# Kernel optimization log

Measured on AMD Instinct MI355X. Metric: run time of the kernel, lower is better.

## Reference

```python
import jax, jax.numpy as jnp
import numpy as np

# Fixed geometry from the module's voxel_dict
VOXEL = np.array([0.32, 0.32, 6.0], dtype=np.float32)
PC_MIN = np.array([-74.88, -74.88, -2.0], dtype=np.float32)
PC_MAX = np.array([74.88, 74.88, 4.0], dtype=np.float32)
NX, NY, NZ = 468, 468, 1          # round((max-min)/voxel) per axis
CANVAS = NZ * NY * NX             # 219024 voxels (batch_size = 1)
OFFSET = VOXEL / 2.0 + PC_MIN     # x/y/z_offset from __init__


def setup_inputs() -> dict:
    key = jax.random.key(0)
    k1, k2, k3, k4 = jax.random.split(key, 4)
    N = 400000
    # points uniformly inside the point-cloud range (dynamic voxelization keeps all)
    xyz = jax.random.uniform(k1, (N, 3), dtype=jnp.float32) * (PC_MAX - PC_MIN) * 0.999 + PC_MIN
    extra = jax.random.normal(k2, (N, 2), dtype=jnp.float32)
    points = jnp.concatenate([xyz, extra], axis=1)          # [N, 5]
    W1 = jax.random.normal(k3, (11, 64), dtype=jnp.float32) * 0.05
    W2 = jax.random.normal(k4, (128, 64), dtype=jnp.float32) * 0.05
    return {"points": points, "W1": W1, "W2": W2}


def _flat_voxel_index(xyz):
    # dynamic voxelization: integer voxel coord per point, (z, y, x) ordering
    c = jnp.floor((xyz - PC_MIN) / VOXEL).astype(jnp.int32)
    cx = jnp.clip(c[:, 0], 0, NX - 1)
    cy = jnp.clip(c[:, 1], 0, NY - 1)
    cz = jnp.clip(c[:, 2], 0, NZ - 1)
    flat = cz * (NY * NX) + cy * NX + cx                    # canvas index as in map_voxel_center_to_point
    return flat, cx, cy, cz


def reference(points, W1, W2):
    xyz = points[:, :3]
    flat, cx, cy, cz = _flat_voxel_index(xyz)

    # DynamicScatter mean (cluster_scatter)
    cnt = jax.ops.segment_sum(jnp.ones((points.shape[0],), jnp.float32), flat, num_segments=CANVAS)
    vsum = jax.ops.segment_sum(points, flat, num_segments=CANVAS)
    vmean = vsum / jnp.maximum(cnt, 1.0)[:, None]           # [CANVAS, 5]
    pmean = vmean[flat]                                     # gather voxel mean to points

    f_cluster = xyz - pmean[:, :3]
    centers = jnp.stack([cx, cy, cz], axis=1).astype(jnp.float32) * VOXEL + OFFSET
    f_center = xyz - centers
    features = jnp.concatenate([points, f_cluster, f_center], axis=-1)   # [N, 11]

    occ = (cnt > 0)[:, None]

    # PFN layer 1: Linear(bias=False) + ReLU, then scatter-max to voxels
    pf1 = jax.nn.relu(features @ W1)                        # [N, 64]
    v1 = jax.ops.segment_max(pf1, flat, num_segments=CANVAS)
    v1 = jnp.where(occ, v1, 0.0)                            # zero empty voxels (replaces -inf)

    # gather voxel max back to points, concat, PFN layer 2
    feat2 = jnp.concatenate([pf1, v1[flat]], axis=1)        # [N, 128]
    pf2 = jax.nn.relu(feat2 @ W2)                           # [N, 64]
    v2 = jax.ops.segment_max(pf2, flat, num_segments=CANVAS)
    v2 = jnp.where(occ, v2, 0.0)                            # [CANVAS, 64] dense voxel features
    return v2
```

## Files before the change

kernel.cpp:

```cpp
#include <hip/hip_runtime.h>

#define NXc 468
#define NYc 468
#define CANVASc (468 * 468)
#define NPTS 400000
#define RUN 16
#define NRUNS (NPTS / RUN)
#define GPTS ((NPTS + 255) / 256)
#define GVOX ((CANVASc + 255) / 256)
#define GBND (NRUNS / 4)

#define PCMIN_X (-74.88f)
#define PCMIN_Y (-74.88f)
#define VOX_X 0.32f
#define VOX_Y 0.32f
#define OFF_X (-74.72f)
#define OFF_Y (-74.72f)
#define OFF_Z (1.0f)

typedef __attribute__((ext_vector_type(8))) short v8s;
typedef __attribute__((ext_vector_type(4))) float v4f;

static_assert(sizeof(__bf16) == 2, "bf16 must be 2 bytes");

__device__ __forceinline__ int rli(int x, int p) {
    return __builtin_amdgcn_readlane(x, p);
}
__device__ __forceinline__ float rlf(float x, int p) {
    return __int_as_float(__builtin_amdgcn_readlane(__float_as_int(x), p));
}

__device__ __forceinline__ void split8(const float* f, v8s& h, v8s& l) {
    #pragma unroll
    for (int i = 0; i < 8; i += 2) {
        __bf16 h0 = (__bf16)f[i];
        __bf16 h1 = (__bf16)f[i + 1];
        h[i]     = __builtin_bit_cast(short, h0);
        h[i + 1] = __builtin_bit_cast(short, h1);
        float l0 = f[i]     - (float)h0;
        float l1 = f[i + 1] - (float)h1;
        l[i]     = __builtin_bit_cast(short, (__bf16)l0);
        l[i + 1] = __builtin_bit_cast(short, (__bf16)l1);
    }
}

__device__ __forceinline__ int voxel_cell(float x, float y, int& cx, int& cy) {
    cx = (int)floorf((x - PCMIN_X) / VOX_X);
    cy = (int)floorf((y - PCMIN_Y) / VOX_Y);
    cx = min(max(cx, 0), NXc - 1);
    cy = min(max(cy, 0), NYc - 1);
    return cy * NXc + cx;
}

__device__ __forceinline__ void kw_body(int tid,
                                        const float* __restrict__ W1,
                                        const float* __restrict__ W2,
                                        v8s* __restrict__ w1frag,
                                        v8s* __restrict__ w2frag) {
    if (tid < 1024) {
        int f = tid >> 6, lane = tid & 63;
        int t = f >> 2, c = f & 3;
        int q = lane >> 4, n = lane & 15;
        float v[8];
        #pragma unroll
        for (int i = 0; i < 8; i++) v[i] = W2[(c * 32 + q * 8 + i) * 64 + t * 16 + n];
        v8s h, l;
        split8(v, h, l);
        w2frag[(f * 2 + 0) * 64 + lane] = h;
        w2frag[(f * 2 + 1) * 64 + lane] = l;
    } else if (tid < 1280) {
        int f = (tid - 1024) >> 6, lane = (tid - 1024) & 63;
        int q = lane >> 4, n = lane & 15;
        float v[8];
        #pragma unroll
        for (int i = 0; i < 8; i++) {
            int k = q * 8 + i;
            v[i] = (k < 11) ? W1[k * 64 + f * 16 + n] : 0.f;
        }
        v8s h, l;
        split8(v, h, l);
        w1frag[(f * 2 + 0) * 64 + lane] = h;
        w1frag[(f * 2 + 1) * 64 + lane] = l;
    }
}

__global__ __launch_bounds__(256) void k_stats(const float* __restrict__ pts,
                                               int* __restrict__ cnt,
                                               int* __restrict__ rankb,
                                               int* __restrict__ cellu,
                                               const float* __restrict__ W1,
                                               const float* __restrict__ W2,
                                               v8s* __restrict__ w1frag,
                                               v8s* __restrict__ w2frag) {
    int b = blockIdx.x;
    if (b >= GPTS) {
        kw_body((b - GPTS) * 256 + threadIdx.x, W1, W2, w1frag, w2frag);
        return;
    }
    int i = b * 256 + threadIdx.x;
    if (i >= NPTS) return;
    float x = pts[i * 5 + 0], y = pts[i * 5 + 1];
    int cx, cy;
    int fl = voxel_cell(x, y, cx, cy);
    rankb[i] = atomicAdd(&cnt[fl], 1);
    cellu[i] = cx | (cy << 16);
}

__global__ __launch_bounds__(256) void k_alloc(const int* __restrict__ cnt,
                                               int* __restrict__ cursor,
                                               int* __restrict__ gcur) {
    int v = blockIdx.x * 256 + threadIdx.x;
    int lane = threadIdx.x & 63;
    int c = (v < CANVASc) ? cnt[v] : 0;
    int scan = c;
    #pragma unroll
    for (int off = 1; off < 64; off <<= 1) {
        int t = __shfl_up(scan, off, 64);
        if (lane >= off) scan += t;
    }
    int total = __shfl(scan, 63, 64);
    int base = 0;
    if (lane == 0 && total > 0) base = atomicAdd(gcur, total);
    base = __shfl(base, 0, 64);
    if (v < CANVASc) cursor[v] = base + scan - c;
}

__device__ __forceinline__ void gather_pt(const float* __restrict__ pts, int pi,
                                          float4& A, float& e1) {
    const float* pp = pts + (size_t)pi * 5;
    __builtin_memcpy(&A, pp, 16);
    e1 = pp[4];
}

__global__ __launch_bounds__(256) void k_scatter(const float* __restrict__ pts,
                                                 const int* __restrict__ cursor,
                                                 const int* __restrict__ rankb,
                                                 const int* __restrict__ cellu,
                                                 float4* __restrict__ pos4,
                                                 float* __restrict__ e1b,
                                                 int* __restrict__ cellb) {
    int i = blockIdx.x * 256 + threadIdx.x;
    if (i >= NPTS) return;
    float4 A; float e1;
    gather_pt(pts, i, A, e1);
    int cell = cellu[i];
    int cx = cell & 0xFFFF, cy = cell >> 16;
    int fl = cy * NXc + cx;
    int pos = cursor[fl] + rankb[i];
    pos4[pos] = A;
    e1b[pos] = e1;
    cellb[pos] = cell;
}

__global__ __launch_bounds__(256) void kV(const int* __restrict__ cnt,
                                          const int* __restrict__ cursor,
                                          const float4* __restrict__ pos4,
                                          const float* __restrict__ e1b,
                                          const int* __restrict__ cellb,
                                          const float* __restrict__ W1,
                                          float4* __restrict__ vmean4,
                                          float* __restrict__ v1c,
                                          float* __restrict__ out) {
    int b = blockIdx.x;
    if (b >= GVOX) {
        int j = threadIdx.x & 63;
        int wslot = threadIdx.x >> 6;
        int w = (b - GVOX) * 4 + wslot;
        if (w == 0 || w >= NRUNS) return;
        int bb = w * RUN;
        int ca = cellb[bb - 1], cb0 = cellb[bb];
        if (ca != cb0) return;
        int cx = ca & 0xFFFF, cy = ca >> 16;
        int v = cy * NXc + cx;
        int c = cnt[v];
        int start = cursor[v];
        out[(size_t)v * 64 + j] = 0.f;

        float sx = 0.f, sy = 0.f, sz = 0.f;
        for (int pb = 0; pb < c; pb += 64) {
            int pc = min(c - pb, 64);
            if (j < pc) {
                float4 A = pos4[start + pb + j];
                sx += A.x; sy += A.y; sz += A.z;
            }
        }
        #pragma unroll
        for (int off = 1; off < 64; off <<= 1) {
            sx += __shfl_xor(sx, off, 64);
            sy += __shfl_xor(sy, off, 64);
            sz += __shfl_xor(sz, off, 64);
        }
        float inv = 1.0f / (float)c;
        float mx = sx * inv, my = sy * inv, mz = sz * inv;

        float wgt[11];
        #pragma unroll
        for (int k = 0; k < 11; k++) wgt[k] = W1[k * 64 + j];
        float vmax = 0.f;
        for (int pb = 0; pb < c; pb += 64) {
            int pc = min(c - pb, 64);
            float f[11];
            #pragma unroll
            for (int k = 0; k < 11; k++) f[k] = 0.f;
            if (j < pc) {
                int idx = start + pb + j;
                float4 A = pos4[idx];
                float e1 = e1b[idx];
                int cell = cellb[idx];
                int ccx = cell & 0xFFFF, ccy = cell >> 16;
                f[0] = A.x; f[1] = A.y; f[2] = A.z; f[3] = A.w; f[4] = e1;
                f[5] = A.x - mx; f[6] = A.y - my; f[7] = A.z - mz;
                f[8] = A.x - (ccx * VOX_X + OFF_X);
                f[9] = A.y - (ccy * VOX_Y + OFF_Y);
                f[10] = A.z - OFF_Z;
            }
            for (int p = 0; p < pc; p++) {
                float acc = 0.f;
                #pragma unroll
                for (int k = 0; k < 11; k++)
                    acc = fmaf(rlf(f[k], p), wgt[k], acc);
                vmax = fmaxf(vmax, acc);
            }
        }
        v1c[(size_t)w * 64 + j] = vmax;
        return;
    }
    int v = b * 256 + threadIdx.x;
    if (v >= CANVASc) return;
    int c = cnt[v];
    if (c == 0) {
        float4 z = make_float4(0.f, 0.f, 0.f, 0.f);
        float4* o = (float4*)out + (size_t)v * 16;
        #pragma unroll
        for (int i = 0; i < 16; i++) o[i] = z;
        return;
    }
    int start = cursor[v];
    float sx = 0.f, sy = 0.f, sz = 0.f;
    for (int i = 0; i < c; i++) {
        float4 p = pos4[start + i];
        sx += p.x; sy += p.y; sz += p.z;
    }
    float inv = 1.0f / (float)c;
    vmean4[v] = make_float4(sx * inv, sy * inv, sz * inv, 0.f);
}

struct PtRegs {
    float4 A;
    float  e1, fcx, fcy, fcz;
    float  mx, my, mz;
    int    vx;
};
__device__ __forceinline__ PtRegs load_pt(const float4* __restrict__ pos4,
                                          const float* __restrict__ e1b,
                                          const int* __restrict__ cellb,
                                          const float4* __restrict__ vmean4,
                                          int base, int j) {
    PtRegs r;
    r.A = make_float4(0.f, 0.f, 0.f, 0.f);
    r.e1 = r.fcx = r.fcy = r.fcz = r.mx = r.my = r.mz = 0.f;
    r.vx = -1;
    int idx = -1;
    if (j < RUN) idx = base + j;
    else if (j == 16) idx = (base + RUN < NPTS) ? base + RUN : -1;
    else if (j == 17) idx = base - 1;
    if (idx >= 0) {
        int cell = cellb[idx];
        int cx = cell & 0xFFFF, cy = cell >> 16;
        int vv = cy * NXc + cx;
        r.vx = vv;
        if (j < RUN) {
            float4 A = pos4[idx];
            r.A = A;
            r.e1 = e1b[idx];
            r.fcx = A.x - (cx * VOX_X + OFF_X);
            r.fcy = A.y - (cy * VOX_Y + OFF_Y);
            r.fcz = A.z - OFF_Z;
            float4 m = vmean4[vv];
            r.mx = m.x; r.my = m.y; r.mz = m.z;
        }
    }
    return r;
}

#define PSTR 68

__device__ __forceinline__ void phase1_mfma(float (*s_pf)[PSTR], const PtRegs& P,
                                            const v8s* __restrict__ w1frag, int j) {
    if (j < RUN) {
        float* row = s_pf[j];
        row[0] = P.A.x; row[1] = P.A.y; row[2] = P.A.z; row[3] = P.A.w; row[4] = P.e1;
        row[5] = P.A.x - P.mx; row[6] = P.A.y - P.my; row[7] = P.A.z - P.mz;
        row[8] = P.fcx; row[9] = P.fcy; row[10] = P.fcz;
        #pragma unroll
        for (int t = 11; t < 16; t++) row[t] = 0.f;
    }
    __builtin_amdgcn_wave_barrier();

    const int m = j & 15, q = j >> 4;
    v8s fh = {0,0,0,0,0,0,0,0}, fl_ = {0,0,0,0,0,0,0,0};
    if (q < 2) {
        float f8[8];
        #pragma unroll
        for (int i = 0; i < 8; i++) f8[i] = s_pf[m][q * 8 + i];
        split8(f8, fh, fl_);
    }
    v4f d[4];
    #pragma unroll
    for (int t = 0; t < 4; t++) {
        v8s bh = w1frag[(t * 2 + 0) * 64 + j];
        v8s bl = w1frag[(t * 2 + 1) * 64 + j];
        v4f acc = {0.f, 0.f, 0.f, 0.f};
        acc = __builtin_amdgcn_mfma_f32_16x16x32_bf16(fh,  bh, acc, 0, 0, 0);
        acc = __builtin_amdgcn_mfma_f32_16x16x32_bf16(fl_, bh, acc, 0, 0, 0);
        acc = __builtin_amdgcn_mfma_f32_16x16x32_bf16(fh,  bl, acc, 0, 0, 0);
        d[t] = acc;
    }
    __builtin_amdgcn_wave_barrier();
    #pragma unroll
    for (int t = 0; t < 4; t++)
        #pragma unroll
        for (int r = 0; r < 4; r++)
            s_pf[q * 4 + r][t * 16 + m] = fmaxf(d[t][r], 0.f);
    __builtin_amdgcn_wave_barrier();
}

__global__ __launch_bounds__(256) void kB(const float4* __restrict__ pos4,
                                          const float* __restrict__ e1b,
                                          const int* __restrict__ cellb,
                                          const float4* __restrict__ vmean4,
                                          const v8s* __restrict__ w1frag,
                                          const v8s* __restrict__ w2frag,
                                          const float* __restrict__ v1c,
                                          float* __restrict__ out) {
    __shared__ float s_pf[4][RUN][PSTR];
    int wslot = threadIdx.x >> 6;
    int wave = blockIdx.x * 4 + wslot;
    int j = threadIdx.x & 63;
    int base = wave * RUN;

    PtRegs P = load_pt(pos4, e1b, cellb, vmean4, base, j);

    const int m = j & 15, q = j >> 4;

    const int first = rli(P.vx, 0), last = rli(P.vx, RUN - 1);
    const bool firstExt = (rli(P.vx, 17) == first);
    const bool lastExt  = (rli(P.vx, 16) == last);

    int vx_m = __builtin_amdgcn_ds_bpermute(m << 2, P.vx);
    int vx_prev = __shfl_up(P.vx, 1, 64);
    unsigned long long B =
        __ballot((j < RUN) && ((j == 0) || (P.vx != vx_prev)));
    int s_seg = 63 - __builtin_clzll(B & ((2ULL << m) - 1ULL));
    int e_seg = m + 1 + (int)__builtin_ctzll((B | (1ULL << RUN)) >> (m + 1));
    const bool fext_m = (vx_m == first && firstExt);
    const bool ext_m = fext_m || (vx_m == last && lastExt);
    const int bidx = fext_m ? wave : (wave + 1);

    phase1_mfma(s_pf[wslot], P, w1frag, j);

    float vf[16];
    if (ext_m) {
        const float* vr = v1c + (size_t)bidx * 64 + q * 8;
        #pragma unroll
        for (int c = 0; c < 2; c++)
            #pragma unroll
            for (int i = 0; i < 8; i++) vf[c * 8 + i] = vr[c * 32 + i];
    }

    v8s ah[4], al[4];
    #pragma unroll
    for (int c = 0; c < 2; c++) {
        float f[8];
        #pragma unroll
        for (int i = 0; i < 8; i++) f[i] = s_pf[wslot][m][c * 32 + q * 8 + i];
        split8(f, ah[c], al[c]);
    }
    if (!ext_m) {
        #pragma unroll
        for (int i = 0; i < 16; i++) vf[i] = 0.f;
        for (int p = s_seg; p < e_seg; p++) {
            const float* row = s_pf[wslot][p];
            float4 a0 = *(const float4*)&row[q * 8];
            float4 a1 = *(const float4*)&row[q * 8 + 4];
            float4 b0 = *(const float4*)&row[32 + q * 8];
            float4 b1 = *(const float4*)&row[32 + q * 8 + 4];
            vf[0] = fmaxf(vf[0], a0.x);  vf[1] = fmaxf(vf[1], a0.y);
            vf[2] = fmaxf(vf[2], a0.z);  vf[3] = fmaxf(vf[3], a0.w);
            vf[4] = fmaxf(vf[4], a1.x);  vf[5] = fmaxf(vf[5], a1.y);
            vf[6] = fmaxf(vf[6], a1.z);  vf[7] = fmaxf(vf[7], a1.w);
            vf[8] = fmaxf(vf[8], b0.x);  vf[9] = fmaxf(vf[9], b0.y);
            vf[10] = fmaxf(vf[10], b0.z); vf[11] = fmaxf(vf[11], b0.w);
            vf[12] = fmaxf(vf[12], b1.x); vf[13] = fmaxf(vf[13], b1.y);
            vf[14] = fmaxf(vf[14], b1.z); vf[15] = fmaxf(vf[15], b1.w);
        }
    }
    split8(vf + 0, ah[2], al[2]);
    split8(vf + 8, ah[3], al[3]);
    __builtin_amdgcn_wave_barrier();

    #pragma unroll
    for (int t = 0; t < 4; t++) {
        v8s bh[4], bl[4];
        #pragma unroll
        for (int c = 0; c < 4; c++) {
            bh[c] = w2frag[((t * 4 + c) * 2 + 0) * 64 + j];
            bl[c] = w2frag[((t * 4 + c) * 2 + 1) * 64 + j];
        }
        v4f acc = {0.f, 0.f, 0.f, 0.f};
        #pragma unroll
        for (int c = 0; c < 4; c++) {
            acc = __builtin_amdgcn_mfma_f32_16x16x32_bf16(ah[c], bh[c], acc, 0, 0, 0);
            acc = __builtin_amdgcn_mfma_f32_16x16x32_bf16(al[c], bh[c], acc, 0, 0, 0);
            acc = __builtin_amdgcn_mfma_f32_16x16x32_bf16(ah[c], bl[c], acc, 0, 0, 0);
        }
        #pragma unroll
        for (int r = 0; r < 4; r++) s_pf[wslot][q * 4 + r][t * 16 + m] = acc[r];
    }
    __builtin_amdgcn_wave_barrier();

    int vprev = first;
    float smax = -3.4e38f;
    for (int p = 0; p < RUN; p++) {
        int vp = rli(P.vx, p);
        if (vp != vprev) {
            float r = fmaxf(smax, 0.f);
            size_t o = (size_t)vprev * 64 + j;
            bool ua = (vprev == first && firstExt) || (vprev == last && lastExt);
            if (ua) atomicMax((int*)out + o, __float_as_int(r));
            else out[o] = r;
            vprev = vp; smax = -3.4e38f;
        }
        smax = fmaxf(smax, s_pf[wslot][p][j]);
    }
    {
        float r = fmaxf(smax, 0.f);
        size_t o = (size_t)vprev * 64 + j;
        bool ua = (vprev == first && firstExt) || (vprev == last && lastExt);
        if (ua) atomicMax((int*)out + o, __float_as_int(r));
        else out[o] = r;
    }
}

extern "C" void kernel_launch(void* const* d_in, const int* in_sizes, int n_in,
                              void* d_out, int out_size, void* d_ws, size_t ws_size,
                              hipStream_t stream) {
    const float* pts = (const float*)d_in[0];
    const float* W1  = (const float*)d_in[1];
    const float* W2  = (const float*)d_in[2];
    float* out = (float*)d_out;

    float4* vmean4 = (float4*)d_ws;
    float*  v1c    = (float*)(vmean4 + CANVASc);
    float4* pos4   = (float4*)(v1c + (size_t)NRUNS * 64);
    float*  e1b    = (float*)(pos4 + NPTS);
    int*    cellb  = (int*)(e1b + NPTS);
    int*    rankb  = cellb + NPTS;
    int*    cellu  = rankb + NPTS;
    v8s*    w2frag = (v8s*)(cellu + NPTS);
    v8s*    w1frag = w2frag + 2048;
    int*    cnt    = (int*)(w1frag + 512);
    int*    gcur   = cnt + CANVASc;
    int*    cursor = gcur + 1;

    hipMemsetAsync(cnt, 0, (size_t)(CANVASc + 1) * 4, stream);

    k_stats  <<<GPTS + 5, 256, 0, stream>>>(pts, cnt, rankb, cellu,
                                            W1, W2, w1frag, w2frag);
    k_alloc  <<<GVOX, 256, 0, stream>>>(cnt, cursor, gcur);
    k_scatter<<<GPTS, 256, 0, stream>>>(pts, cursor, rankb, cellu,
                                        pos4, e1b, cellb);
    kV       <<<GVOX + GBND, 256, 0, stream>>>(cnt, cursor, pos4, e1b, cellb,
                                               W1, vmean4, v1c, out);
    kB       <<<NRUNS / 4, 256, 0, stream>>>(pos4, e1b, cellb, vmean4, w1frag,
                                             w2frag, v1c, out);
}
```

Measured before the change: 221.8 us.

## Compute voxel means in-wave in kB and move empty-voxel zeroing into k_alloc

The per-voxel mean pass over the whole canvas is removed. kB now computes each voxel's mean from the run's points using wave shuffles over segment bounds. Only voxels that span run boundaries get their mean precomputed, by the boundary kernel, into a small per-run buffer. Zeroing of empty voxels' output moves into k_alloc, so the old kV kernel shrinks to a boundary-only kernel. This removes a canvas-wide read/write of vmean4 and a random gather, in exchange for extra shuffle work in kB.

```diff
diff --git a/kernel.cpp b/kernel.cpp
--- a/kernel.cpp
+++ b/kernel.cpp
@@ -108,7 +108,8 @@
 
 __global__ __launch_bounds__(256) void k_alloc(const int* __restrict__ cnt,
                                                int* __restrict__ cursor,
-                                               int* __restrict__ gcur) {
+                                               int* __restrict__ gcur,
+                                               float4* __restrict__ out4) {
     int v = blockIdx.x * 256 + threadIdx.x;
     int lane = threadIdx.x & 63;
     int c = (v < CANVASc) ? cnt[v] : 0;
@@ -122,7 +123,15 @@
     int base = 0;
     if (lane == 0 && total > 0) base = atomicAdd(gcur, total);
     base = __shfl(base, 0, 64);
-    if (v < CANVASc) cursor[v] = base + scan - c;
+    if (v < CANVASc) {
+        cursor[v] = base + scan - c;
+        if (c == 0) {
+            float4 z = make_float4(0.f, 0.f, 0.f, 0.f);
+            float4* o = out4 + (size_t)v * 16;
+            #pragma unroll
+            for (int i = 0; i < 16; i++) o[i] = z;
+        }
+    }
 }
 
 __device__ __forceinline__ void gather_pt(const float* __restrict__ pts, int pi,
@@ -152,97 +161,76 @@
     cellb[pos] = cell;
 }
 
-__global__ __launch_bounds__(256) void kV(const int* __restrict__ cnt,
+__global__ __launch_bounds__(256) void kS(const int* __restrict__ cnt,
                                           const int* __restrict__ cursor,
                                           const float4* __restrict__ pos4,
                                           const float* __restrict__ e1b,
                                           const int* __restrict__ cellb,
                                           const float* __restrict__ W1,
-                                          float4* __restrict__ vmean4,
+                                          float4* __restrict__ vmc,
                                           float* __restrict__ v1c,
                                           float* __restrict__ out) {
-    int b = blockIdx.x;
-    if (b >= GVOX) {
-        int j = threadIdx.x & 63;
-        int wslot = threadIdx.x >> 6;
-        int w = (b - GVOX) * 4 + wslot;
-        if (w == 0 || w >= NRUNS) return;
-        int bb = w * RUN;
-        int ca = cellb[bb - 1], cb0 = cellb[bb];
-        if (ca != cb0) return;
-        int cx = ca & 0xFFFF, cy = ca >> 16;
-        int v = cy * NXc + cx;
-        int c = cnt[v];
-        int start = cursor[v];
-        out[(size_t)v * 64 + j] = 0.f;
-
-        float sx = 0.f, sy = 0.f, sz = 0.f;
-        for (int pb = 0; pb < c; pb += 64) {
-            int pc = min(c - pb, 64);
-            if (j < pc) {
-                float4 A = pos4[start + pb + j];
-                sx += A.x; sy += A.y; sz += A.z;
-            }
-        }
-        #pragma unroll
-        for (int off = 1; off < 64; off <<= 1) {
-            sx += __shfl_xor(sx, off, 64);
-            sy += __shfl_xor(sy, off, 64);
-            sz += __shfl_xor(sz, off, 64);
-        }
-        float inv = 1.0f / (float)c;
-        float mx = sx * inv, my = sy * inv, mz = sz * inv;
-
-        float wgt[11];
-        #pragma unroll
-        for (int k = 0; k < 11; k++) wgt[k] = W1[k * 64 + j];
-        float vmax = 0.f;
-        for (int pb = 0; pb < c; pb += 64) {
-            int pc = min(c - pb, 64);
-            float f[11];
+    int j = threadIdx.x & 63;
+    int wslot = threadIdx.x >> 6;
+    int w = blockIdx.x * 4 + wslot;
+    if (w == 0 || w >= NRUNS) return;
+    int bb = w * RUN;
+    int ca = cellb[bb - 1], cb0 = cellb[bb];
+    if (ca != cb0) return;
+    int cx = ca & 0xFFFF, cy = ca >> 16;
+    int v = cy * NXc + cx;
+    int c = cnt[v];
+    int start = cursor[v];
+    out[(size_t)v * 64 + j] = 0.f;
+
+    float sx = 0.f, sy = 0.f, sz = 0.f;
+    for (int pb = 0; pb < c; pb += 64) {
+        int pc = min(c - pb, 64);
+        if (j < pc) {
+            float4 A = pos4[start + pb + j];
+            sx += A.x; sy += A.y; sz += A.z;
+        }
+    }
+    #pragma unroll
+    for (int off = 1; off < 64; off <<= 1) {
+        sx += __shfl_xor(sx, off, 64);
+        sy += __shfl_xor(sy, off, 64);
+        sz += __shfl_xor(sz, off, 64);
+    }
+    float inv = 1.0f / (float)c;
+    float mx = sx * inv, my = sy * inv, mz = sz * inv;
+    if (j == 0) vmc[w] = make_float4(mx, my, mz, 0.f);
+
+    float wgt[11];
+    #pragma unroll
+    for (int k = 0; k < 11; k++) wgt[k] = W1[k * 64 + j];
+    float vmax = 0.f;
+    for (int pb = 0; pb < c; pb += 64) {
+        int pc = min(c - pb, 64);
+        float f[11];
+        #pragma unroll
+        for (int k = 0; k < 11; k++) f[k] = 0.f;
+        if (j < pc) {
+            int idx = start + pb + j;
+            float4 A = pos4[idx];
+            float e1 = e1b[idx];
+            int cell = cellb[idx];
+            int ccx = cell & 0xFFFF, ccy = cell >> 16;
+            f[0] = A.x; f[1] = A.y; f[2] = A.z; f[3] = A.w; f[4] = e1;
+            f[5] = A.x - mx; f[6] = A.y - my; f[7] = A.z - mz;
+            f[8] = A.x - (ccx * VOX_X + OFF_X);
+            f[9] = A.y - (ccy * VOX_Y + OFF_Y);
+            f[10] = A.z - OFF_Z;
+        }
+        for (int p = 0; p < pc; p++) {
+            float acc = 0.f;
             #pragma unroll
-            for (int k = 0; k < 11; k++) f[k] = 0.f;
-            if (j < pc) {
-                int idx = start + pb + j;
-                float4 A = pos4[idx];
-                float e1 = e1b[idx];
-                int cell = cellb[idx];
-                int ccx = cell & 0xFFFF, ccy = cell >> 16;
-                f[0] = A.x; f[1] = A.y; f[2] = A.z; f[3] = A.w; f[4] = e1;
-                f[5] = A.x - mx; f[6] = A.y - my; f[7] = A.z - mz;
-                f[8] = A.x - (ccx * VOX_X + OFF_X);
-                f[9] = A.y - (ccy * VOX_Y + OFF_Y);
-                f[10] = A.z - OFF_Z;
-            }
-            for (int p = 0; p < pc; p++) {
-                float acc = 0.f;
-                #pragma unroll
-                for (int k = 0; k < 11; k++)
-                    acc = fmaf(rlf(f[k], p), wgt[k], acc);
-                vmax = fmaxf(vmax, acc);
-            }
-        }
-        v1c[(size_t)w * 64 + j] = vmax;
-        return;
-    }
-    int v = b * 256 + threadIdx.x;
-    if (v >= CANVASc) return;
-    int c = cnt[v];
-    if (c == 0) {
-        float4 z = make_float4(0.f, 0.f, 0.f, 0.f);
-        float4* o = (float4*)out + (size_t)v * 16;
-        #pragma unroll
-        for (int i = 0; i < 16; i++) o[i] = z;
-        return;
-    }
-    int start = cursor[v];
-    float sx = 0.f, sy = 0.f, sz = 0.f;
-    for (int i = 0; i < c; i++) {
-        float4 p = pos4[start + i];
-        sx += p.x; sy += p.y; sz += p.z;
-    }
-    float inv = 1.0f / (float)c;
-    vmean4[v] = make_float4(sx * inv, sy * inv, sz * inv, 0.f);
+            for (int k = 0; k < 11; k++)
+                acc = fmaf(rlf(f[k], p), wgt[k], acc);
+            vmax = fmaxf(vmax, acc);
+        }
+    }
+    v1c[(size_t)w * 64 + j] = vmax;
 }
 
 struct PtRegs {
@@ -251,37 +239,6 @@
     float  mx, my, mz;
     int    vx;
 };
-__device__ __forceinline__ PtRegs load_pt(const float4* __restrict__ pos4,
-                                          const float* __restrict__ e1b,
-                                          const int* __restrict__ cellb,
-                                          const float4* __restrict__ vmean4,
-                                          int base, int j) {
-    PtRegs r;
-    r.A = make_float4(0.f, 0.f, 0.f, 0.f);
-    r.e1 = r.fcx = r.fcy = r.fcz = r.mx = r.my = r.mz = 0.f;
-    r.vx = -1;
-    int idx = -1;
-    if (j < RUN) idx = base + j;
-    else if (j == 16) idx = (base + RUN < NPTS) ? base + RUN : -1;
-    else if (j == 17) idx = base - 1;
-    if (idx >= 0) {
-        int cell = cellb[idx];
-        int cx = cell & 0xFFFF, cy = cell >> 16;
-        int vv = cy * NXc + cx;
-        r.vx = vv;
-        if (j < RUN) {
-            float4 A = pos4[idx];
-            r.A = A;
-            r.e1 = e1b[idx];
-            r.fcx = A.x - (cx * VOX_X + OFF_X);
-            r.fcy = A.y - (cy * VOX_Y + OFF_Y);
-            r.fcz = A.z - OFF_Z;
-            float4 m = vmean4[vv];
-            r.mx = m.x; r.my = m.y; r.mz = m.z;
-        }
-    }
-    return r;
-}
 
 #define PSTR 68
 
@@ -328,7 +285,7 @@
 __global__ __launch_bounds__(256) void kB(const float4* __restrict__ pos4,
                                           const float* __restrict__ e1b,
                                           const int* __restrict__ cellb,
-                                          const float4* __restrict__ vmean4,
+                                          const float4* __restrict__ vmc,
                                           const v8s* __restrict__ w1frag,
                                           const v8s* __restrict__ w2frag,
                                           const float* __restrict__ v1c,
@@ -339,23 +296,58 @@
     int j = threadIdx.x & 63;
     int base = wave * RUN;
 
-    PtRegs P = load_pt(pos4, e1b, cellb, vmean4, base, j);
-
     const int m = j & 15, q = j >> 4;
 
-    const int first = rli(P.vx, 0), last = rli(P.vx, RUN - 1);
-    const bool firstExt = (rli(P.vx, 17) == first);
-    const bool lastExt  = (rli(P.vx, 16) == last);
-
-    int vx_m = __builtin_amdgcn_ds_bpermute(m << 2, P.vx);
-    int vx_prev = __shfl_up(P.vx, 1, 64);
+    int idx = -1;
+    if (j < RUN) idx = base + j;
+    else if (j == 16) idx = (base + RUN < NPTS) ? base + RUN : -1;
+    else if (j == 17) idx = base - 1;
+
+    int cell = 0, vx = -1;
+    if (idx >= 0) {
+        cell = cellb[idx];
+        vx = (cell >> 16) * NXc + (cell & 0xFFFF);
+    }
+    float4 A = make_float4(0.f, 0.f, 0.f, 0.f);
+    float e1 = 0.f;
+    if (j < RUN) { A = pos4[idx]; e1 = e1b[idx]; }
+
+    const int first = rli(vx, 0), last = rli(vx, RUN - 1);
+    const bool firstExt = (rli(vx, 17) == first);
+    const bool lastExt  = (rli(vx, 16) == last);
+
+    int vx_m = __builtin_amdgcn_ds_bpermute(m << 2, vx);
+    int vx_prev = __shfl_up(vx, 1, 64);
     unsigned long long B =
-        __ballot((j < RUN) && ((j == 0) || (P.vx != vx_prev)));
+        __ballot((j < RUN) && ((j == 0) || (vx != vx_prev)));
     int s_seg = 63 - __builtin_clzll(B & ((2ULL << m) - 1ULL));
     int e_seg = m + 1 + (int)__builtin_ctzll((B | (1ULL << RUN)) >> (m + 1));
     const bool fext_m = (vx_m == first && firstExt);
     const bool ext_m = fext_m || (vx_m == last && lastExt);
     const int bidx = fext_m ? wave : (wave + 1);
+
+    PtRegs P;
+    P.A = A; P.e1 = e1; P.vx = vx;
+    P.mx = P.my = P.mz = P.fcx = P.fcy = P.fcz = 0.f;
+    if (j < RUN) {
+        if (ext_m) {
+            float4 mv = vmc[bidx];
+            P.mx = mv.x; P.my = mv.y; P.mz = mv.z;
+        } else {
+            float sx = 0.f, sy = 0.f, sz = 0.f;
+            for (int p = s_seg; p < e_seg; p++) {
+                sx += __shfl(A.x, p, 64);
+                sy += __shfl(A.y, p, 64);
+                sz += __shfl(A.z, p, 64);
+            }
+            float inv = 1.0f / (float)(e_seg - s_seg);
+            P.mx = sx * inv; P.my = sy * inv; P.mz = sz * inv;
+        }
+        int cx = cell & 0xFFFF, cy = cell >> 16;
+        P.fcx = A.x - (cx * VOX_X + OFF_X);
+        P.fcy = A.y - (cy * VOX_Y + OFF_Y);
+        P.fcz = A.z - OFF_Z;
+    }
 
     phase1_mfma(s_pf[wslot], P, w1frag, j);
 
@@ -422,7 +414,7 @@
     int vprev = first;
     float smax = -3.4e38f;
     for (int p = 0; p < RUN; p++) {
-        int vp = rli(P.vx, p);
+        int vp = rli(vx, p);
         if (vp != vprev) {
             float r = fmaxf(smax, 0.f);
             size_t o = (size_t)vprev * 64 + j;
@@ -450,8 +442,8 @@
     const float* W2  = (const float*)d_in[2];
     float* out = (float*)d_out;
 
-    float4* vmean4 = (float4*)d_ws;
-    float*  v1c    = (float*)(vmean4 + CANVASc);
+    float4* vmc    = (float4*)d_ws;
+    float*  v1c    = (float*)(vmc + NRUNS);
     float4* pos4   = (float4*)(v1c + (size_t)NRUNS * 64);
     float*  e1b    = (float*)(pos4 + NPTS);
     int*    cellb  = (int*)(e1b + NPTS);
@@ -467,11 +459,11 @@
 
     k_stats  <<<GPTS + 5, 256, 0, stream>>>(pts, cnt, rankb, cellu,
                                             W1, W2, w1frag, w2frag);
-    k_alloc  <<<GVOX, 256, 0, stream>>>(cnt, cursor, gcur);
+    k_alloc  <<<GVOX, 256, 0, stream>>>(cnt, cursor, gcur, (float4*)out);
     k_scatter<<<GPTS, 256, 0, stream>>>(pts, cursor, rankb, cellu,
                                         pos4, e1b, cellb);
-    kV       <<<GVOX + GBND, 256, 0, stream>>>(cnt, cursor, pos4, e1b, cellb,
-                                               W1, vmean4, v1c, out);
-    kB       <<<NRUNS / 4, 256, 0, stream>>>(pos4, e1b, cellb, vmean4, w1frag,
+    kS       <<<GBND, 256, 0, stream>>>(cnt, cursor, pos4, e1b, cellb,
+                                        W1, vmc, v1c, out);
+    kB       <<<NRUNS / 4, 256, 0, stream>>>(pos4, e1b, cellb, vmc, w1frag,
                                              w2frag, v1c, out);
 }
```

Result: no change. 223.4 us (+0.7%).
